# Performance work log

Measured on AMD Instinct MI355X. Metric: run time of the kernel, lower is better.

The kernel has to match this reference:

```python
import jax, jax.numpy as jnp
import numpy as np

G = 128      # voxel grid extent per axis
N = 300000   # number of occupied input voxels
CIN = 32
COUT = 64

_FILTER = np.array([[-1, -1, -1], [-1, -1, 0], [-1, 0, -1], [-1, 0, 0],
                    [0, -1, -1], [0, -1, 0], [0, 0, -1], [0, 0, 0]], dtype=np.int64)


def calculate_grid(in_pos):
    # faithful numpy port of the torch calculate_grid (returns even integer coords;
    # the actual out position is coord + 0.5)
    out = (in_pos[:, None, :].astype(np.int64) + _FILTER[None, :, :]).reshape(-1, 3)
    out = out[out.min(axis=1) >= 0]
    out = out[~((out % 2).astype(bool).any(axis=1))]
    out = np.unique(out, axis=0)
    return out  # [M, 3] even ints


def setup_inputs() -> dict:
    key = jax.random.key(0)
    k1, k2 = jax.random.split(key)
    rng = np.random.default_rng(0)
    lin = rng.choice(G ** 3, size=N, replace=False)  # unique voxel coords
    pos = np.stack(np.unravel_index(lin, (G, G, G)), axis=1).astype(np.int32)
    features = jax.random.normal(k1, (N, CIN), dtype=jnp.float32)
    weight = jax.random.normal(k2, (2, 2, 2, CIN, COUT), dtype=jnp.float32) * 0.05
    return {"features": features, "in_positions": jnp.asarray(pos), "weight": weight}


def reference(features, in_positions, weight):
    pos = np.asarray(in_positions)            # concrete int coords (constants)
    out_int = calculate_grid(pos)             # [M, 3] even ints; out pos = out_int + 0.5

    # dense voxel-hash: grid cell -> input row index (-1 = empty)
    p = jnp.asarray(pos)
    idx_grid = jnp.full((G, G, G), -1, dtype=jnp.int32)
    idx_grid = idx_grid.at[p[:, 0], p[:, 1], p[:, 2]].set(
        jnp.arange(p.shape[0], dtype=jnp.int32))

    # 2x2x2 kernel, offset=-0.5: kernel index per axis = in_coord - even_out_coord in {0,1}
    offsets = np.stack(np.meshgrid(np.arange(2), np.arange(2), np.arange(2),
                                   indexing='ij'), axis=-1).reshape(8, 3)
    nbs = jnp.asarray(out_int[None, :, :] + offsets[:, None, :])   # [8, M, 3]
    idx = idx_grid[nbs[..., 0], nbs[..., 1], nbs[..., 2]]          # [8, M]
    valid = idx >= 0
    gathered = jnp.where(valid[..., None],
                         features[jnp.maximum(idx, 0)], 0.0)       # [8, M, CIN]
    w = weight.reshape(8, CIN, COUT)
    out_feat = jnp.einsum('kmc,kcf->mf', gathered, w)              # [M, COUT]

    out_positions = (jnp.asarray(out_int, dtype=jnp.float32) + 0.5) / 2.0
    return out_feat, out_positions
```

## Files before the change

### kernel.cpp

```cpp
#include <hip/hip_runtime.h>

#define GFINE 128
#define GC 64
#define NCELLS (GC * GC * GC)
#define CIN 32
#define COUT 64

typedef __attribute__((ext_vector_type(8))) short bf16x8;
typedef __attribute__((ext_vector_type(4))) float f32x4;

__device__ __forceinline__ short f2bf(float f) {
    union { float f; unsigned u; } v; v.f = f;
    unsigned r = v.u + 0x7fffu + ((v.u >> 16) & 1u);
    return (short)(r >> 16);
}

#define TAB_OFF   0u
#define OCC_OFF   8388608u
#define CL_OFF    9437184u
#define BS_OFF    10485760u
#define WSWZ_OFF  10489856u

__global__ void setup_kernel(const float* __restrict__ w, char* __restrict__ ws) {
    int bid = blockIdx.x, tid = threadIdx.x;
    if (bid < 256) {
        ((int4*)(ws + OCC_OFF))[bid * 256 + tid] = make_int4(0, 0, 0, 0);
    } else {
        int t = (bid - 256) * 256 + tid;
        int lane = t & 63, cb = (t >> 6) & 3, k = t >> 8;
        bf16x8 o;
#pragma unroll
        for (int e = 0; e < 8; ++e)
            o[e] = f2bf(w[(k * CIN + ((lane >> 4) * 8 + e)) * COUT + cb * 16 + (lane & 15)]);
        ((bf16x8*)(ws + WSWZ_OFF))[t] = o;
    }
}

__global__ void scatter_kernel(const int* __restrict__ pos, int n,
                               int* __restrict__ tab, int* __restrict__ occ) {
    int i = blockIdx.x * blockDim.x + threadIdx.x;
    if (i >= n) return;
    int x = pos[i * 3 + 0];
    int y = pos[i * 3 + 1];
    int z = pos[i * 3 + 2];
    int cell = ((x >> 1) * GC + (y >> 1)) * GC + (z >> 1);
    int k = ((x & 1) << 2) | ((y & 1) << 1) | (z & 1);
    tab[cell * 8 + k] = i;
    atomicOr(&occ[cell], 1 << k);
}

__global__ __launch_bounds__(256) void sum_kernel(const int* __restrict__ occ,
                                                  int* __restrict__ blockSums) {
    __shared__ int lds[256];
    int tid = threadIdx.x, bid = blockIdx.x;
    int4 o = ((const int4*)occ)[bid * 256 + tid];
    lds[tid] = (o.x != 0) + (o.y != 0) + (o.z != 0) + (o.w != 0);
    __syncthreads();
    for (int off = 128; off > 0; off >>= 1) {
        if (tid < off) lds[tid] += lds[tid + off];
        __syncthreads();
    }
    if (tid == 0) blockSums[bid] = lds[0];
}

__global__ __launch_bounds__(256) void compact_kernel(
    const int* __restrict__ occ, const int* __restrict__ blockSums,
    int* __restrict__ cellList, float* __restrict__ out_pos) {
    __shared__ int lds[256], ldsb[256];
    int tid = threadIdx.x, bid = blockIdx.x;
    int4 o = ((const int4*)occ)[bid * 256 + tid];
    int c0 = (o.x != 0), c1 = (o.y != 0), c2 = (o.z != 0), c3 = (o.w != 0);
    int s = c0 + c1 + c2 + c3;
    lds[tid] = s;
    ldsb[tid] = blockSums[tid];
    __syncthreads();
    for (int off = 1; off < 256; off <<= 1) {
        int t  = (tid >= off) ? lds[tid - off]  : 0;
        int tb = (tid >= off) ? ldsb[tid - off] : 0;
        __syncthreads();
        lds[tid]  += t;
        ldsb[tid] += tb;
        __syncthreads();
    }
    int excl_block = bid ? ldsb[bid - 1] : 0;
    int rank = excl_block + lds[tid] - s;
    int cellBase = (bid * 256 + tid) * 4;
    int oc[4] = {o.x, o.y, o.z, o.w};
#pragma unroll
    for (int c = 0; c < 4; ++c) {
        if (oc[c]) {
            int cell = cellBase + c;
            cellList[rank] = cell | (oc[c] << 18);
            int cx = cell >> 12, cy = (cell >> 6) & 63, cz = cell & 63;
            out_pos[rank * 3 + 0] = cx + 0.25f;
            out_pos[rank * 3 + 1] = cy + 0.25f;
            out_pos[rank * 3 + 2] = cz + 0.25f;
            ++rank;
        }
    }
}

__global__ __launch_bounds__(256) void conv_kernel(
    const float* __restrict__ feat, const short* __restrict__ wswz,
    const int* __restrict__ tab, const int* __restrict__ cellList,
    int M, float* __restrict__ out_feat) {
    const int lane = threadIdx.x & 63;
    const int wv = threadIdx.x >> 6;
    const int base = (blockIdx.x * 4 + wv) * 16;
    if (base >= M) return;
    const int cslot = lane & 15;
    const int tgrp  = lane >> 4;

    int rank = base + cslot;
    if (rank >= M) rank = M - 1;
    int e = cellList[rank];
    int cell = e & 0x3FFFF;
    int occ8 = (e >> 18) & 0xFF;

    const int4* tp = (const int4*)(tab + cell * 8);
    int4 t0 = tp[0], t1 = tp[1];
    int rr[8] = {t0.x, t0.y, t0.z, t0.w, t1.x, t1.y, t1.z, t1.w};

    float4 u[8], v[8];
#pragma unroll
    for (int k = 0; k < 8; ++k) {
        if ((occ8 >> k) & 1) {
            const float4* fr = (const float4*)(feat + (size_t)rr[k] * CIN + tgrp * 8);
            u[k] = fr[0];
            v[k] = fr[1];
        }
    }

    const bf16x8* wf = (const bf16x8*)wswz;
    f32x4 acc0 = {0.f, 0.f, 0.f, 0.f}, acc1 = acc0, acc2 = acc0, acc3 = acc0;
#pragma unroll
    for (int k = 0; k < 8; ++k) {
        bf16x8 a = {0, 0, 0, 0, 0, 0, 0, 0};
        if ((occ8 >> k) & 1) {
            a[0] = f2bf(u[k].x); a[1] = f2bf(u[k].y);
            a[2] = f2bf(u[k].z); a[3] = f2bf(u[k].w);
            a[4] = f2bf(v[k].x); a[5] = f2bf(v[k].y);
            a[6] = f2bf(v[k].z); a[7] = f2bf(v[k].w);
        }
        acc0 = __builtin_amdgcn_mfma_f32_16x16x32_bf16(a, wf[(k * 4 + 0) * 64 + lane], acc0, 0, 0, 0);
        acc1 = __builtin_amdgcn_mfma_f32_16x16x32_bf16(a, wf[(k * 4 + 1) * 64 + lane], acc1, 0, 0, 0);
        acc2 = __builtin_amdgcn_mfma_f32_16x16x32_bf16(a, wf[(k * 4 + 2) * 64 + lane], acc2, 0, 0, 0);
        acc3 = __builtin_amdgcn_mfma_f32_16x16x32_bf16(a, wf[(k * 4 + 3) * 64 + lane], acc3, 0, 0, 0);
    }

#pragma unroll
    for (int i = 0; i < 4; ++i) {
        int row = base + tgrp * 4 + i;
        if (row < M) {
            float* o = out_feat + (size_t)row * COUT + cslot;
            o[0]  = acc0[i];
            o[16] = acc1[i];
            o[32] = acc2[i];
            o[48] = acc3[i];
        }
    }
}

extern "C" void kernel_launch(void* const* d_in, const int* in_sizes, int n_in,
                              void* d_out, int out_size, void* d_ws, size_t ws_size,
                              hipStream_t stream) {
    const float* feat   = (const float*)d_in[0];
    const int*   pos    = (const int*)d_in[1];
    const float* weight = (const float*)d_in[2];
    int n = in_sizes[1] / 3;
    int M = out_size / 67;

    char* ws = (char*)d_ws;
    int* tab        = (int*)(ws + TAB_OFF);
    int* occ        = (int*)(ws + OCC_OFF);
    int* cellList   = (int*)(ws + CL_OFF);
    int* blockSums  = (int*)(ws + BS_OFF);
    short* wswz     = (short*)(ws + WSWZ_OFF);

    float* out_feat = (float*)d_out;
    float* out_pos  = (float*)d_out + (size_t)M * COUT;

    setup_kernel<<<264, 256, 0, stream>>>(weight, ws);
    scatter_kernel<<<(n + 255) / 256, 256, 0, stream>>>(pos, n, tab, occ);
    sum_kernel<<<256, 256, 0, stream>>>(occ, blockSums);
    compact_kernel<<<256, 256, 0, stream>>>(occ, blockSums, cellList, out_pos);
    conv_kernel<<<(M + 63) / 64, 256, 0, stream>>>(feat, wswz, tab, cellList,
                                                   M, out_feat);
}
```

Measured before the change: 59.19 us.

## Pre-sort features into cell-contiguous bf16 buffer and drop dense index table

Replaces the dense 8-slot per-cell index table with a per-cell prefix of occupied inputs, computed by counting popcounts in the scan. A new scatter pass converts each input feature row to bf16 and writes it into a compacted buffer ordered by output cell, so the conv kernel reads contiguous bf16 rows instead of gathering scattered fp32 rows. The aim is to cut gather traffic and to take the conversion out of the conv kernel. In exchange it adds an extra kernel launch and a full pass that reads and rewrites the features.

```diff
diff --git a/kernel.cpp b/kernel.cpp
--- a/kernel.cpp
+++ b/kernel.cpp
@@ -15,13 +15,15 @@
     return (short)(r >> 16);
 }
 
-#define TAB_OFF   0u
-#define OCC_OFF   8388608u
-#define CL_OFF    9437184u
-#define BS_OFF    10485760u
-#define WSWZ_OFF  10489856u
-
-__global__ void setup_kernel(const float* __restrict__ w, char* __restrict__ ws) {
+#define OCC_OFF   0u
+#define RG_OFF    1048576u
+#define META_OFF  2097152u
+#define BS_OFF    3145728u
+#define WSWZ_OFF  3149824u
+#define GFEAT_OFF 4194304u
+
+__global__ __launch_bounds__(256) void setup_kernel(const float* __restrict__ w,
+                                                    char* __restrict__ ws) {
     int bid = blockIdx.x, tid = threadIdx.x;
     if (bid < 256) {
         ((int4*)(ws + OCC_OFF))[bid * 256 + tid] = make_int4(0, 0, 0, 0);
@@ -36,8 +38,8 @@
     }
 }
 
-__global__ void scatter_kernel(const int* __restrict__ pos, int n,
-                               int* __restrict__ tab, int* __restrict__ occ) {
+__global__ __launch_bounds__(256) void scatter1_kernel(const int* __restrict__ pos,
+                                                       int n, int* __restrict__ occ) {
     int i = blockIdx.x * blockDim.x + threadIdx.x;
     if (i >= n) return;
     int x = pos[i * 3 + 0];
@@ -45,65 +47,99 @@
     int z = pos[i * 3 + 2];
     int cell = ((x >> 1) * GC + (y >> 1)) * GC + (z >> 1);
     int k = ((x & 1) << 2) | ((y & 1) << 1) | (z & 1);
-    tab[cell * 8 + k] = i;
     atomicOr(&occ[cell], 1 << k);
 }
 
 __global__ __launch_bounds__(256) void sum_kernel(const int* __restrict__ occ,
-                                                  int* __restrict__ blockSums) {
+                                                  int2* __restrict__ blockSums) {
     __shared__ int lds[256];
     int tid = threadIdx.x, bid = blockIdx.x;
     int4 o = ((const int4*)occ)[bid * 256 + tid];
-    lds[tid] = (o.x != 0) + (o.y != 0) + (o.z != 0) + (o.w != 0);
+    int s = (o.x != 0) + (o.y != 0) + (o.z != 0) + (o.w != 0);
+    int h = __builtin_popcount(o.x) + __builtin_popcount(o.y) +
+            __builtin_popcount(o.z) + __builtin_popcount(o.w);
+    lds[tid] = (h << 16) | s;
     __syncthreads();
     for (int off = 128; off > 0; off >>= 1) {
         if (tid < off) lds[tid] += lds[tid + off];
         __syncthreads();
     }
-    if (tid == 0) blockSums[bid] = lds[0];
+    if (tid == 0) blockSums[bid] = make_int2(lds[0] & 0xFFFF, lds[0] >> 16);
 }
 
 __global__ __launch_bounds__(256) void compact_kernel(
-    const int* __restrict__ occ, const int* __restrict__ blockSums,
-    int* __restrict__ cellList, float* __restrict__ out_pos) {
-    __shared__ int lds[256], ldsb[256];
+    const int* __restrict__ occ, const int2* __restrict__ blockSums,
+    int* __restrict__ meta, int* __restrict__ rank_grid,
+    float* __restrict__ out_pos) {
+    __shared__ int lds[256];
+    __shared__ unsigned long long ldsb[256];
     int tid = threadIdx.x, bid = blockIdx.x;
     int4 o = ((const int4*)occ)[bid * 256 + tid];
-    int c0 = (o.x != 0), c1 = (o.y != 0), c2 = (o.z != 0), c3 = (o.w != 0);
-    int s = c0 + c1 + c2 + c3;
-    lds[tid] = s;
-    ldsb[tid] = blockSums[tid];
+    int oc[4] = {o.x, o.y, o.z, o.w};
+    int s = (o.x != 0) + (o.y != 0) + (o.z != 0) + (o.w != 0);
+    int h = __builtin_popcount(o.x) + __builtin_popcount(o.y) +
+            __builtin_popcount(o.z) + __builtin_popcount(o.w);
+    lds[tid] = (h << 16) | s;
+    int2 bs = blockSums[tid];
+    ldsb[tid] = ((unsigned long long)bs.y << 32) | (unsigned)bs.x;
     __syncthreads();
     for (int off = 1; off < 256; off <<= 1) {
-        int t  = (tid >= off) ? lds[tid - off]  : 0;
-        int tb = (tid >= off) ? ldsb[tid - off] : 0;
+        int t = (tid >= off) ? lds[tid - off] : 0;
+        unsigned long long tb = (tid >= off) ? ldsb[tid - off] : 0ull;
         __syncthreads();
-        lds[tid]  += t;
+        lds[tid] += t;
         ldsb[tid] += tb;
         __syncthreads();
     }
-    int excl_block = bid ? ldsb[bid - 1] : 0;
-    int rank = excl_block + lds[tid] - s;
+    unsigned long long g = bid ? ldsb[bid - 1] : 0ull;
+    int incl = lds[tid];
+    int rank    = (int)(g & 0xFFFFFFFFull) + (incl & 0xFFFF) - s;
+    int hitBase = (int)(g >> 32) + (incl >> 16) - h;
     int cellBase = (bid * 256 + tid) * 4;
-    int oc[4] = {o.x, o.y, o.z, o.w};
 #pragma unroll
     for (int c = 0; c < 4; ++c) {
         if (oc[c]) {
             int cell = cellBase + c;
-            cellList[rank] = cell | (oc[c] << 18);
+            int mv = (hitBase << 8) | oc[c];
+            meta[rank] = mv;
+            rank_grid[cell] = mv;
             int cx = cell >> 12, cy = (cell >> 6) & 63, cz = cell & 63;
             out_pos[rank * 3 + 0] = cx + 0.25f;
             out_pos[rank * 3 + 1] = cy + 0.25f;
             out_pos[rank * 3 + 2] = cz + 0.25f;
             ++rank;
+            hitBase += __builtin_popcount(oc[c]);
         }
     }
 }
 
+__global__ __launch_bounds__(256) void scatter2_kernel(
+    const int* __restrict__ pos, const float* __restrict__ feat, int n,
+    const int* __restrict__ rank_grid, short* __restrict__ gfeat) {
+    int i = blockIdx.x * blockDim.x + threadIdx.x;
+    if (i >= n) return;
+    int x = pos[i * 3 + 0];
+    int y = pos[i * 3 + 1];
+    int z = pos[i * 3 + 2];
+    int cell = ((x >> 1) * GC + (y >> 1)) * GC + (z >> 1);
+    int k = ((x & 1) << 2) | ((y & 1) << 1) | (z & 1);
+    int mg = rank_grid[cell];
+    int dest = (mg >> 8) + __builtin_popcount(mg & ((1 << k) - 1));
+    const float4* fr = (const float4*)(feat + (size_t)i * CIN);
+    bf16x8* gp = (bf16x8*)gfeat + dest * 4;
+#pragma unroll
+    for (int q = 0; q < 4; ++q) {
+        float4 a = fr[2 * q], b = fr[2 * q + 1];
+        bf16x8 o;
+        o[0] = f2bf(a.x); o[1] = f2bf(a.y); o[2] = f2bf(a.z); o[3] = f2bf(a.w);
+        o[4] = f2bf(b.x); o[5] = f2bf(b.y); o[6] = f2bf(b.z); o[7] = f2bf(b.w);
+        gp[q] = o;
+    }
+}
+
 __global__ __launch_bounds__(256) void conv_kernel(
-    const float* __restrict__ feat, const short* __restrict__ wswz,
-    const int* __restrict__ tab, const int* __restrict__ cellList,
-    int M, float* __restrict__ out_feat) {
+    const short* __restrict__ gfeat, const short* __restrict__ wswz,
+    const int* __restrict__ meta, int M, float* __restrict__ out_feat) {
     const int lane = threadIdx.x & 63;
     const int wv = threadIdx.x >> 6;
     const int base = (blockIdx.x * 4 + wv) * 16;
@@ -113,39 +149,30 @@
 
     int rank = base + cslot;
     if (rank >= M) rank = M - 1;
-    int e = cellList[rank];
-    int cell = e & 0x3FFFF;
-    int occ8 = (e >> 18) & 0xFF;
-
-    const int4* tp = (const int4*)(tab + cell * 8);
-    int4 t0 = tp[0], t1 = tp[1];
-    int rr[8] = {t0.x, t0.y, t0.z, t0.w, t1.x, t1.y, t1.z, t1.w};
-
-    float4 u[8], v[8];
+    int mg = meta[rank];
+    int hb = mg >> 8;
+    int occ8 = mg & 0xFF;
+
+    const bf16x8* gf = (const bf16x8*)gfeat;
+    const bf16x8 zero = {0, 0, 0, 0, 0, 0, 0, 0};
+    bf16x8 a[8];
 #pragma unroll
     for (int k = 0; k < 8; ++k) {
-        if ((occ8 >> k) & 1) {
-            const float4* fr = (const float4*)(feat + (size_t)rr[k] * CIN + tgrp * 8);
-            u[k] = fr[0];
-            v[k] = fr[1];
-        }
+        int bit = (occ8 >> k) & 1;
+        int row = hb + __builtin_popcount(occ8 & ((1 << k) - 1));
+        row = bit ? row : 0;
+        bf16x8 t = gf[row * 4 + tgrp];
+        a[k] = bit ? t : zero;
     }
 
     const bf16x8* wf = (const bf16x8*)wswz;
     f32x4 acc0 = {0.f, 0.f, 0.f, 0.f}, acc1 = acc0, acc2 = acc0, acc3 = acc0;
 #pragma unroll
     for (int k = 0; k < 8; ++k) {
-        bf16x8 a = {0, 0, 0, 0, 0, 0, 0, 0};
-        if ((occ8 >> k) & 1) {
-            a[0] = f2bf(u[k].x); a[1] = f2bf(u[k].y);
-            a[2] = f2bf(u[k].z); a[3] = f2bf(u[k].w);
-            a[4] = f2bf(v[k].x); a[5] = f2bf(v[k].y);
-            a[6] = f2bf(v[k].z); a[7] = f2bf(v[k].w);
-        }
-        acc0 = __builtin_amdgcn_mfma_f32_16x16x32_bf16(a, wf[(k * 4 + 0) * 64 + lane], acc0, 0, 0, 0);
-        acc1 = __builtin_amdgcn_mfma_f32_16x16x32_bf16(a, wf[(k * 4 + 1) * 64 + lane], acc1, 0, 0, 0);
-        acc2 = __builtin_amdgcn_mfma_f32_16x16x32_bf16(a, wf[(k * 4 + 2) * 64 + lane], acc2, 0, 0, 0);
-        acc3 = __builtin_amdgcn_mfma_f32_16x16x32_bf16(a, wf[(k * 4 + 3) * 64 + lane], acc3, 0, 0, 0);
+        acc0 = __builtin_amdgcn_mfma_f32_16x16x32_bf16(a[k], wf[(k * 4 + 0) * 64 + lane], acc0, 0, 0, 0);
+        acc1 = __builtin_amdgcn_mfma_f32_16x16x32_bf16(a[k], wf[(k * 4 + 1) * 64 + lane], acc1, 0, 0, 0);
+        acc2 = __builtin_amdgcn_mfma_f32_16x16x32_bf16(a[k], wf[(k * 4 + 2) * 64 + lane], acc2, 0, 0, 0);
+        acc3 = __builtin_amdgcn_mfma_f32_16x16x32_bf16(a[k], wf[(k * 4 + 3) * 64 + lane], acc3, 0, 0, 0);
     }
 
 #pragma unroll
@@ -171,19 +198,20 @@
     int M = out_size / 67;
 
     char* ws = (char*)d_ws;
-    int* tab        = (int*)(ws + TAB_OFF);
-    int* occ        = (int*)(ws + OCC_OFF);
-    int* cellList   = (int*)(ws + CL_OFF);
-    int* blockSums  = (int*)(ws + BS_OFF);
-    short* wswz     = (short*)(ws + WSWZ_OFF);
+    int*   occ       = (int*)(ws + OCC_OFF);
+    int*   rank_grid = (int*)(ws + RG_OFF);
+    int*   meta      = (int*)(ws + META_OFF);
+    int2*  blockSums = (int2*)(ws + BS_OFF);
+    short* wswz      = (short*)(ws + WSWZ_OFF);
+    short* gfeat     = (short*)(ws + GFEAT_OFF);
 
     float* out_feat = (float*)d_out;
     float* out_pos  = (float*)d_out + (size_t)M * COUT;
 
     setup_kernel<<<264, 256, 0, stream>>>(weight, ws);
-    scatter_kernel<<<(n + 255) / 256, 256, 0, stream>>>(pos, n, tab, occ);
+    scatter1_kernel<<<(n + 255) / 256, 256, 0, stream>>>(pos, n, occ);
     sum_kernel<<<256, 256, 0, stream>>>(occ, blockSums);
-    compact_kernel<<<256, 256, 0, stream>>>(occ, blockSums, cellList, out_pos);
-    conv_kernel<<<(M + 63) / 64, 256, 0, stream>>>(feat, wswz, tab, cellList,
-                                                   M, out_feat);
-}
+    compact_kernel<<<256, 256, 0, stream>>>(occ, blockSums, meta, rank_grid, out_pos);
+    scatter2_kernel<<<(n + 255) / 256, 256, 0, stream>>>(pos, feat, n, rank_grid, gfeat);
+    conv_kernel<<<(M + 63) / 64, 256, 0, stream>>>(gfeat, wswz, meta, M, out_feat);
+}
```

Result: slower. 67.55 us (+14.1%).
